# Kernel tuning notes

Measured on AMD Instinct MI355X. Metric: run time of the kernel, lower is better.

Reference implementation:

```python
import jax, jax.numpy as jnp
import numpy as np

E, T, D = 100000, 400000, 128
LN_EPS = 1e-5


def setup_inputs() -> dict:
    key = jax.random.key(0)
    k1, k2, k3 = jax.random.split(key, 3)
    f_edge = jax.random.normal(k1, (E, D), dtype=jnp.float32)
    W = jax.random.normal(k2, (3 * D, D), dtype=jnp.float32) / np.sqrt(3 * D)
    b = jnp.zeros((D,), dtype=jnp.float32)
    gamma = jnp.ones((D,), dtype=jnp.float32)
    beta = jnp.zeros((D,), dtype=jnp.float32)
    triangle = jax.random.randint(k3, (T, 3), 0, E, dtype=jnp.int64)
    return {"f_edge": f_edge, "W": W, "b": b, "gamma": gamma, "beta": beta,
            "triangle": triangle}


def reference(f_edge, W, b, gamma, beta, triangle):
    # f_edge [E, D], triangle [T, 3] -> gather to [T, 3, D], flatten to [T, 3D]
    t = triangle.shape[0]
    e, d = f_edge.shape
    f_tri = f_edge[triangle].reshape(t, 3 * d)
    # Linear(3D -> D) + exact GELU (torch nn.GELU default is erf-based)
    h = jax.nn.gelu(f_tri @ W + b, approximate=False)  # [T, D]
    # scatter_mean over destination edge index triangle[:, 2], dim_size=E
    dst = triangle[:, 2]
    seg_sum = jax.ops.segment_sum(h, dst, num_segments=e)            # [E, D]
    cnt = jax.ops.segment_sum(jnp.ones((t,), h.dtype), dst, num_segments=e)
    mean = seg_sum / jnp.maximum(cnt, 1.0)[:, None]
    # dropout is identity in eval mode; LayerNorm over last dim
    mu = jnp.mean(mean, axis=-1, keepdims=True)
    var = jnp.mean(jnp.square(mean - mu), axis=-1, keepdims=True)
    return (mean - mu) / jnp.sqrt(var + LN_EPS) * gamma + beta
```

## Files before the change

### kernel.cpp

```cpp
#include <hip/hip_runtime.h>
#include <hip/hip_bf16.h>

typedef __attribute__((ext_vector_type(8))) short short8;
typedef __attribute__((ext_vector_type(4))) float floatx4;
typedef __attribute__((ext_vector_type(4))) unsigned int uintx4;

__device__ __forceinline__ float gelu_fast(float x)
{
    float u = 0.7978845608f * x * (1.0f + 0.044715f * x * x);
    float e = __builtin_amdgcn_exp2f(2.885390082f * u);
    return x - x * __builtin_amdgcn_rcpf(e + 1.0f);
}

__global__ __launch_bounds__(256)
void prep(const float* __restrict__ Wg, uintx4* __restrict__ wq,
          const int* __restrict__ tri, int* __restrict__ cnt,
          int* __restrict__ slot, int T)
{
    int g = blockIdx.x * 256 + threadIdx.x;
    if (g < T) {
        int i2 = tri[g * 3 + 2];
        slot[g] = atomicAdd(&cnt[i2], 1);
    } else {
        int i = g - T;
        if (i < 6144) {
            int frag = i >> 6, lane = i & 63;
            int ko = frag >> 3, nt = frag & 7;
            int col = lane & 15, quad = lane >> 4;
            unsigned short tmp[8] __attribute__((aligned(16)));
#pragma unroll
            for (int j = 0; j < 8; ++j) {
                __hip_bfloat16 b =
                    __float2bfloat16(Wg[(ko * 32 + quad * 8 + j) * 128 + nt * 16 + col]);
                tmp[j] = *(unsigned short*)&b;
            }
            wq[i] = *(const uintx4*)tmp;
        }
    }
}

__device__ __forceinline__ int wave_incl_scan(int v, int lane)
{
#pragma unroll
    for (int o = 1; o < 64; o <<= 1) {
        int u = __shfl_up(v, o);
        if (lane >= o) v += u;
    }
    return v;
}

__global__ __launch_bounds__(1024)
void scan_blk(const int* __restrict__ in, int* __restrict__ outExcl,
              int* __restrict__ partial, int n,
              int* __restrict__ hist, int* __restrict__ histx)
{
    __shared__ int ws[16];
    __shared__ int lh[64];
    int t = threadIdx.x;
    int g = blockIdx.x * 1024 + t;
    int lane = t & 63, wv = t >> 6;
    int v = (g < n) ? in[g] : 0;
    int sc = wave_incl_scan(v, lane);
    if (lane == 63) ws[wv] = sc;
    if (hist && !histx && t < 64) lh[t] = 0;
    __syncthreads();
    if (wv == 0) {
        int b = (lane < 16) ? ws[lane] : 0;
        int bs = wave_incl_scan(b, lane);
        if (lane < 16) ws[lane] = bs;
    }
    if (hist && !histx && g < n) atomicAdd(&lh[v < 63 ? v : 63], 1);
    __syncthreads();
    int off = wv ? ws[wv - 1] : 0;
    if (g < n) outExcl[g] = off + sc - v;
    if (partial && t == 0) partial[blockIdx.x] = ws[15];
    if (hist && !histx && t < 64 && lh[t]) atomicAdd(&hist[t], lh[t]);
    if (histx && t < 64) {
        int hv = hist[t];
        int hs = wave_incl_scan(hv, lane);
        histx[t] = hs - hv;
    }
}

__global__ __launch_bounds__(256)
void scatter(const int* __restrict__ tri, const int* __restrict__ slot,
             const int* __restrict__ excl, const int* __restrict__ pscan,
             const int* __restrict__ cnt, int2* __restrict__ srec,
             const int* __restrict__ histx, int* __restrict__ histcur,
             int2* __restrict__ sinfo, int E, int T)
{
    __shared__ int lcnt[64];
    __shared__ int lbase[64];
    int t = threadIdx.x;
    int g = blockIdx.x * 256 + t;

    if (t < 64) lcnt[t] = 0;
    __syncthreads();

    int cc = 0, lofs = 0, c = 0, start = 0;
    if (g < E) {
        c = cnt[g];
        start = excl[g] + pscan[g >> 10];
        cc = c < 63 ? c : 63;
        lofs = atomicAdd(&lcnt[cc], 1);
    }
    __syncthreads();
    if (t < 64 && lcnt[t]) lbase[t] = atomicAdd(&histcur[t], lcnt[t]);
    __syncthreads();
    if (g < E) {
        int rank = histx[cc] + lbase[cc] + lofs;
        sinfo[rank] = make_int2((start << 8) | (c < 255 ? c : 255), g);
    }

    if (g < T) {
        int i0 = tri[g * 3 + 0];
        int i1 = tri[g * 3 + 1];
        int i2 = tri[g * 3 + 2];
        int pos = excl[i2] + pscan[i2 >> 10] + slot[g];
        srec[pos] = make_int2(i0 << 8, i1 << 8);
    }
    if (g < 8)
        srec[T + g] = make_int2(0, 0);
}

__global__ __launch_bounds__(1024, 1)
void edge_gemm(const float* __restrict__ fe_f, const uintx4* __restrict__ wq,
               unsigned short* __restrict__ G, int E)
{
    __shared__ uintx4 ldsW[6144];

    const int tid  = threadIdx.x;
    const int wv   = tid >> 6;
    const int lane = tid & 63;
    const int col  = lane & 15;
    const int quad = lane >> 4;
    const int ntiles = (E + 15) >> 4;

    for (int i = tid; i < 6144; i += 1024) ldsW[i] = wq[i];
    __syncthreads();

#pragma unroll 1
    for (int tile = blockIdx.x * 16 + wv; tile < ntiles; tile += gridDim.x * 16) {
        int row_a = tile * 16 + col;
        if (row_a >= E) row_a = E - 1;
        const float* arow = fe_f + (size_t)row_a * 128 + quad * 8;

        floatx4 f[8];
#pragma unroll
        for (int l = 0; l < 8; ++l)
            f[l] = *(const floatx4*)(arow + (l >> 1) * 32 + (l & 1) * 4);

        short8 a[4];
#pragma unroll
        for (int ko = 0; ko < 4; ++ko) {
            unsigned short tmp[8] __attribute__((aligned(16)));
#pragma unroll
            for (int j = 0; j < 8; ++j) {
                __hip_bfloat16 b = __float2bfloat16(f[ko * 2 + (j >> 2)][j & 3]);
                tmp[j] = *(unsigned short*)&b;
            }
            a[ko] = *(const short8*)tmp;
        }

#pragma unroll 1
        for (int r = 0; r < 3; ++r) {
            floatx4 acc[8];
#pragma unroll
            for (int nt = 0; nt < 8; ++nt) acc[nt] = (floatx4)0.0f;

#pragma unroll
            for (int ko = 0; ko < 4; ++ko) {
#pragma unroll
                for (int nt = 0; nt < 8; ++nt) {
                    short8 bf = *(const short8*)&ldsW[r * 2048 + (ko * 8 + nt) * 64 + lane];
                    acc[nt] = __builtin_amdgcn_mfma_f32_16x16x32_bf16(a[ko], bf, acc[nt], 0, 0, 0);
                }
            }

            unsigned short* Gr = G + (size_t)r * E * 128;
#pragma unroll
            for (int rr = 0; rr < 4; ++rr) {
                int row = tile * 16 + quad * 4 + rr;
                if (row < E) {
                    unsigned short pk[8] __attribute__((aligned(16)));
#pragma unroll
                    for (int nt = 0; nt < 8; ++nt) {
                        __hip_bfloat16 hb = __float2bfloat16(acc[nt][rr]);
                        pk[nt] = *(unsigned short*)&hb;
                    }
                    *(uintx4*)(Gr + (size_t)row * 128 + col * 8) = *(const uintx4*)pk;
                }
            }
        }
    }
}

__global__ __launch_bounds__(256)
void mean_ln(const unsigned short* __restrict__ G, const int2* __restrict__ sinfo,
             const int* __restrict__ cnt, const int2* __restrict__ srec,
             const float* __restrict__ bias, const float* __restrict__ gamma,
             const float* __restrict__ beta, float* __restrict__ out, int E)
{
    const int tid  = threadIdx.x;
    const int lane = tid & 63;
    const int wid  = tid >> 6;
    const int h    = lane >> 4;
    const int s    = lane & 15;

    const char* g0 = (const char*)G + s * 16;
    const char* g1 = g0 + (size_t)E * 256;
    const char* g2 = g1 + (size_t)E * 256;

    float bv[8], gm[8], bt[8];
#pragma unroll
    for (int k = 0; k < 8; ++k) {
        bv[k] = bias[k * 16 + s];
        gm[k] = gamma[k * 16 + s];
        bt[k] = beta[k * 16 + s];
    }

    const int ngroups = (E + 3) >> 2;
    const int nwaves  = gridDim.x * 4;

    for (int grp = blockIdx.x * 4 + wid; grp < ngroups; grp += nwaves) {
        int rank = grp * 4 + h;
        int rk   = rank < E ? rank : E - 1;

        int2 si  = sinfo[rk];
        int row  = si.y;
        int c    = si.x & 255;
        int start = (int)((unsigned)si.x >> 8);
        if (__builtin_expect(c == 255, 0)) c = cnt[row];

        int cmax = max(c, __shfl_xor(c, 16));
        cmax = max(cmax, __shfl_xor(cmax, 32));

        uintx4 w2 = *(const uintx4*)(g2 + (size_t)row * 256);
        float base[8];
#pragma unroll
        for (int k = 0; k < 8; ++k) {
            unsigned int wv = (k & 1) ? (w2[k >> 1] & 0xffff0000u)
                                      : (w2[k >> 1] << 16);
            base[k] = __uint_as_float(wv) + bv[k];
        }

        float x[8];
#pragma unroll
        for (int k = 0; k < 8; ++k) x[k] = 0.0f;

        int cl = c - 1; if (cl < 0) cl = 0;
        for (int t = 0; t < cmax; t += 4) {
            int ci = t + (s & 3);
            if (ci > cl) ci = cl;
            int2 rr = srec[start + ci];
#pragma unroll
            for (int k = 0; k < 4; ++k) {
                unsigned int o0 = (unsigned)__shfl(rr.x, (h << 4) + k);
                unsigned int o1 = (unsigned)__shfl(rr.y, (h << 4) + k);
                uintx4 a = *(const uintx4*)(g0 + (size_t)o0);
                uintx4 b = *(const uintx4*)(g1 + (size_t)o1);
                bool ok = (t + k) < c;
#pragma unroll
                for (int p = 0; p < 8; ++p) {
                    unsigned int wa = (p & 1) ? (a[p >> 1] & 0xffff0000u)
                                              : (a[p >> 1] << 16);
                    unsigned int wb = (p & 1) ? (b[p >> 1] & 0xffff0000u)
                                              : (b[p >> 1] << 16);
                    float sv = __uint_as_float(wa) + __uint_as_float(wb) + base[p];
                    x[p] += ok ? gelu_fast(sv) : 0.0f;
                }
            }
        }

        float inv = 1.0f / fmaxf((float)c, 1.0f);
        float sm = 0.0f;
#pragma unroll
        for (int k = 0; k < 8; ++k) { x[k] *= inv; sm += x[k]; }
#pragma unroll
        for (int o = 8; o > 0; o >>= 1) sm += __shfl_xor(sm, o);
        float mu = sm * (1.0f / 128.0f);
        float vv = 0.0f;
#pragma unroll
        for (int k = 0; k < 8; ++k) { x[k] -= mu; vv += x[k] * x[k]; }
#pragma unroll
        for (int o = 8; o > 0; o >>= 1) vv += __shfl_xor(vv, o);
        float rstd = rsqrtf(vv * (1.0f / 128.0f) + 1e-5f);

        if (rank < E) {
            float* orow = out + (size_t)row * 128 + s;
#pragma unroll
            for (int k = 0; k < 8; ++k)
                __builtin_nontemporal_store(x[k] * rstd * gm[k] + bt[k],
                                            &orow[k * 16]);
        }
    }
}

extern "C" void kernel_launch(void* const* d_in, const int* in_sizes, int n_in,
                              void* d_out, int out_size, void* d_ws, size_t ws_size,
                              hipStream_t stream)
{
    const float* fe_f  = (const float*)d_in[0];
    const float* Wg    = (const float*)d_in[1];
    const float* bias  = (const float*)d_in[2];
    const float* gamma = (const float*)d_in[3];
    const float* beta  = (const float*)d_in[4];
    const int*   tri   = (const int*)d_in[5];

    int E = in_sizes[0] / 128;
    int T = in_sizes[5] / 3;

    unsigned short* G = (unsigned short*)d_ws;
    int2* srec = (int2*)((char*)d_ws + (size_t)3 * E * 256);
    uintx4* wq = (uintx4*)(srec + T + 8);
    int* slot = (int*)(wq + 6144);
    int* cnt  = slot + T;
    int* hist = cnt + E;
    int* histcur = hist + 64;
    int* histx = histcur + 64;
    int* excl = histx + 64;
    int* partial = excl + E;
    int* pscan = partial + 1024;
    int2* sinfo = (int2*)(pscan + 1024);

    (void)hipMemsetAsync(cnt, 0, (size_t)E * sizeof(int) + 128 * sizeof(int),
                         stream);

    int total = T + 6144;
    prep<<<(total + 255) / 256, 256, 0, stream>>>(Wg, wq, tri, cnt, slot, T);

    int NB = (E + 1023) / 1024;
    scan_blk<<<NB, 1024, 0, stream>>>(cnt, excl, partial, E, hist, nullptr);
    scan_blk<<<1, 1024, 0, stream>>>(partial, pscan, nullptr, NB, hist, histx);

    scatter<<<(T + 255) / 256, 256, 0, stream>>>(tri, slot, excl, pscan, cnt,
                                                 srec, histx, histcur, sinfo,
                                                 E, T);

    edge_gemm<<<256, 1024, 0, stream>>>(fe_f, wq, G, E);

    mean_ln<<<2048, 256, 0, stream>>>(G, sinfo, cnt, srec, bias, gamma, beta,
                                      (float*)d_out, E);
}
```

Measured before the change: 209.5 us.

## Fuse scatter and second-level scan into GEMM launch as extra blocks

Drops the single-block partial-scan kernel and the separate scatter kernel. Their work now runs as extra blocks of the edge GEMM launch, and each of those blocks redoes the small partial and histogram scans locally. This removes two launches and lets the memory-bound scatter overlap with the MFMA-bound GEMM blocks. mean_ln also prefetches the next sinfo entry one iteration ahead and replaces the masked select with an FMA by a 0/1 mask. The cost is redundant small scans in every scatter block and a shared LDS footprint between the two roles.

```diff
diff --git a/kernel.cpp b/kernel.cpp
--- a/kernel.cpp
+++ b/kernel.cpp
@@ -4,6 +4,8 @@
 typedef __attribute__((ext_vector_type(8))) short short8;
 typedef __attribute__((ext_vector_type(4))) float floatx4;
 typedef __attribute__((ext_vector_type(4))) unsigned int uintx4;
+
+#define GEMM_BLOCKS 256
 
 __device__ __forceinline__ float gelu_fast(float x)
 {
@@ -51,8 +53,7 @@
 
 __global__ __launch_bounds__(1024)
 void scan_blk(const int* __restrict__ in, int* __restrict__ outExcl,
-              int* __restrict__ partial, int n,
-              int* __restrict__ hist, int* __restrict__ histx)
+              int* __restrict__ partial, int n, int* __restrict__ hist)
 {
     __shared__ int ws[16];
     __shared__ int lh[64];
@@ -62,136 +63,151 @@
     int v = (g < n) ? in[g] : 0;
     int sc = wave_incl_scan(v, lane);
     if (lane == 63) ws[wv] = sc;
-    if (hist && !histx && t < 64) lh[t] = 0;
+    if (t < 64) lh[t] = 0;
     __syncthreads();
     if (wv == 0) {
         int b = (lane < 16) ? ws[lane] : 0;
         int bs = wave_incl_scan(b, lane);
         if (lane < 16) ws[lane] = bs;
     }
-    if (hist && !histx && g < n) atomicAdd(&lh[v < 63 ? v : 63], 1);
+    if (g < n) atomicAdd(&lh[v < 63 ? v : 63], 1);
     __syncthreads();
     int off = wv ? ws[wv - 1] : 0;
     if (g < n) outExcl[g] = off + sc - v;
-    if (partial && t == 0) partial[blockIdx.x] = ws[15];
-    if (hist && !histx && t < 64 && lh[t]) atomicAdd(&hist[t], lh[t]);
-    if (histx && t < 64) {
-        int hv = hist[t];
-        int hs = wave_incl_scan(hv, lane);
-        histx[t] = hs - hv;
-    }
-}
-
-__global__ __launch_bounds__(256)
-void scatter(const int* __restrict__ tri, const int* __restrict__ slot,
-             const int* __restrict__ excl, const int* __restrict__ pscan,
-             const int* __restrict__ cnt, int2* __restrict__ srec,
-             const int* __restrict__ histx, int* __restrict__ histcur,
-             int2* __restrict__ sinfo, int E, int T)
-{
+    if (t == 0) partial[blockIdx.x] = ws[15];
+    if (t < 64 && lh[t]) atomicAdd(&hist[t], lh[t]);
+}
+
+__global__ __launch_bounds__(1024, 1)
+void gemm_scatter(const float* __restrict__ fe_f, const uintx4* __restrict__ wq,
+                  unsigned short* __restrict__ G, const int* __restrict__ tri,
+                  const int* __restrict__ slot, const int* __restrict__ excl,
+                  const int* __restrict__ partial, const int* __restrict__ hist,
+                  int* __restrict__ histcur, const int* __restrict__ cnt,
+                  int2* __restrict__ srec, int2* __restrict__ sinfo,
+                  int E, int T, int NB)
+{
+    __shared__ uintx4 ldsW[6144];
+    __shared__ int ps[128];
+    __shared__ int hx[64];
+    __shared__ int ws[16];
     __shared__ int lcnt[64];
     __shared__ int lbase[64];
-    int t = threadIdx.x;
-    int g = blockIdx.x * 256 + t;
-
-    if (t < 64) lcnt[t] = 0;
-    __syncthreads();
-
-    int cc = 0, lofs = 0, c = 0, start = 0;
-    if (g < E) {
-        c = cnt[g];
-        start = excl[g] + pscan[g >> 10];
-        cc = c < 63 ? c : 63;
-        lofs = atomicAdd(&lcnt[cc], 1);
-    }
-    __syncthreads();
-    if (t < 64 && lcnt[t]) lbase[t] = atomicAdd(&histcur[t], lcnt[t]);
-    __syncthreads();
-    if (g < E) {
-        int rank = histx[cc] + lbase[cc] + lofs;
-        sinfo[rank] = make_int2((start << 8) | (c < 255 ? c : 255), g);
-    }
-
-    if (g < T) {
-        int i0 = tri[g * 3 + 0];
-        int i1 = tri[g * 3 + 1];
-        int i2 = tri[g * 3 + 2];
-        int pos = excl[i2] + pscan[i2 >> 10] + slot[g];
-        srec[pos] = make_int2(i0 << 8, i1 << 8);
-    }
-    if (g < 8)
-        srec[T + g] = make_int2(0, 0);
-}
-
-__global__ __launch_bounds__(1024, 1)
-void edge_gemm(const float* __restrict__ fe_f, const uintx4* __restrict__ wq,
-               unsigned short* __restrict__ G, int E)
-{
-    __shared__ uintx4 ldsW[6144];
-
-    const int tid  = threadIdx.x;
-    const int wv   = tid >> 6;
-    const int lane = tid & 63;
-    const int col  = lane & 15;
-    const int quad = lane >> 4;
-    const int ntiles = (E + 15) >> 4;
-
-    for (int i = tid; i < 6144; i += 1024) ldsW[i] = wq[i];
-    __syncthreads();
+
+    const int tid = threadIdx.x;
+
+    if (blockIdx.x < GEMM_BLOCKS) {
+        const int wv   = tid >> 6;
+        const int lane = tid & 63;
+        const int col  = lane & 15;
+        const int quad = lane >> 4;
+        const int ntiles = (E + 15) >> 4;
+
+        for (int i = tid; i < 6144; i += 1024) ldsW[i] = wq[i];
+        __syncthreads();
 
 #pragma unroll 1
-    for (int tile = blockIdx.x * 16 + wv; tile < ntiles; tile += gridDim.x * 16) {
-        int row_a = tile * 16 + col;
-        if (row_a >= E) row_a = E - 1;
-        const float* arow = fe_f + (size_t)row_a * 128 + quad * 8;
-
-        floatx4 f[8];
-#pragma unroll
-        for (int l = 0; l < 8; ++l)
-            f[l] = *(const floatx4*)(arow + (l >> 1) * 32 + (l & 1) * 4);
-
-        short8 a[4];
-#pragma unroll
-        for (int ko = 0; ko < 4; ++ko) {
-            unsigned short tmp[8] __attribute__((aligned(16)));
-#pragma unroll
-            for (int j = 0; j < 8; ++j) {
-                __hip_bfloat16 b = __float2bfloat16(f[ko * 2 + (j >> 2)][j & 3]);
-                tmp[j] = *(unsigned short*)&b;
+        for (int tile = blockIdx.x * 16 + wv; tile < ntiles;
+             tile += GEMM_BLOCKS * 16) {
+            int row_a = tile * 16 + col;
+            if (row_a >= E) row_a = E - 1;
+            const float* arow = fe_f + (size_t)row_a * 128 + quad * 8;
+
+            floatx4 f[8];
+#pragma unroll
+            for (int l = 0; l < 8; ++l)
+                f[l] = *(const floatx4*)(arow + (l >> 1) * 32 + (l & 1) * 4);
+
+            short8 a[4];
+#pragma unroll
+            for (int ko = 0; ko < 4; ++ko) {
+                unsigned short tmp[8] __attribute__((aligned(16)));
+#pragma unroll
+                for (int j = 0; j < 8; ++j) {
+                    __hip_bfloat16 b = __float2bfloat16(f[ko * 2 + (j >> 2)][j & 3]);
+                    tmp[j] = *(unsigned short*)&b;
+                }
+                a[ko] = *(const short8*)tmp;
             }
-            a[ko] = *(const short8*)tmp;
-        }
 
 #pragma unroll 1
-        for (int r = 0; r < 3; ++r) {
-            floatx4 acc[8];
-#pragma unroll
-            for (int nt = 0; nt < 8; ++nt) acc[nt] = (floatx4)0.0f;
-
-#pragma unroll
-            for (int ko = 0; ko < 4; ++ko) {
-#pragma unroll
-                for (int nt = 0; nt < 8; ++nt) {
-                    short8 bf = *(const short8*)&ldsW[r * 2048 + (ko * 8 + nt) * 64 + lane];
-                    acc[nt] = __builtin_amdgcn_mfma_f32_16x16x32_bf16(a[ko], bf, acc[nt], 0, 0, 0);
+            for (int r = 0; r < 3; ++r) {
+                floatx4 acc[8];
+#pragma unroll
+                for (int nt = 0; nt < 8; ++nt) acc[nt] = (floatx4)0.0f;
+
+#pragma unroll
+                for (int ko = 0; ko < 4; ++ko) {
+#pragma unroll
+                    for (int nt = 0; nt < 8; ++nt) {
+                        short8 bf = *(const short8*)&ldsW[r * 2048 + (ko * 8 + nt) * 64 + lane];
+                        acc[nt] = __builtin_amdgcn_mfma_f32_16x16x32_bf16(a[ko], bf, acc[nt], 0, 0, 0);
+                    }
+                }
+
+                unsigned short* Gr = G + (size_t)r * E * 128;
+#pragma unroll
+                for (int rr = 0; rr < 4; ++rr) {
+                    int row = tile * 16 + quad * 4 + rr;
+                    if (row < E) {
+                        unsigned short pk[8] __attribute__((aligned(16)));
+#pragma unroll
+                        for (int nt = 0; nt < 8; ++nt) {
+                            __hip_bfloat16 hb = __float2bfloat16(acc[nt][rr]);
+                            pk[nt] = *(unsigned short*)&hb;
+                        }
+                        *(uintx4*)(Gr + (size_t)row * 128 + col * 8) = *(const uintx4*)pk;
+                    }
                 }
             }
-
-            unsigned short* Gr = G + (size_t)r * E * 128;
-#pragma unroll
-            for (int rr = 0; rr < 4; ++rr) {
-                int row = tile * 16 + quad * 4 + rr;
-                if (row < E) {
-                    unsigned short pk[8] __attribute__((aligned(16)));
-#pragma unroll
-                    for (int nt = 0; nt < 8; ++nt) {
-                        __hip_bfloat16 hb = __float2bfloat16(acc[nt][rr]);
-                        pk[nt] = *(unsigned short*)&hb;
-                    }
-                    *(uintx4*)(Gr + (size_t)row * 128 + col * 8) = *(const uintx4*)pk;
-                }
-            }
-        }
+        }
+    } else {
+        const int lane = tid & 63, w = tid >> 6;
+
+        int v = (tid < NB) ? partial[tid] : 0;
+        int sc = wave_incl_scan(v, lane);
+        if (lane == 63) ws[w] = sc;
+        if (tid < 64) lcnt[tid] = 0;
+        __syncthreads();
+        if (w == 0) {
+            int b = (lane < 16) ? ws[lane] : 0;
+            int bs = wave_incl_scan(b, lane);
+            if (lane < 16) ws[lane] = bs;
+            int hv = hist[lane];
+            int hs = wave_incl_scan(hv, lane);
+            hx[lane] = hs - hv;
+        }
+        __syncthreads();
+        int off = w ? ws[w - 1] : 0;
+        if (tid < NB && tid < 128) ps[tid] = off + sc - v;
+        __syncthreads();
+
+        int g = (blockIdx.x - GEMM_BLOCKS) * 1024 + tid;
+
+        int cc = 0, lofs = 0, c = 0, start = 0;
+        if (g < E) {
+            c = cnt[g];
+            start = excl[g] + ps[g >> 10];
+            cc = c < 63 ? c : 63;
+            lofs = atomicAdd(&lcnt[cc], 1);
+        }
+        __syncthreads();
+        if (tid < 64 && lcnt[tid]) lbase[tid] = atomicAdd(&histcur[tid], lcnt[tid]);
+        __syncthreads();
+        if (g < E) {
+            int rank = hx[cc] + lbase[cc] + lofs;
+            sinfo[rank] = make_int2((start << 8) | (c < 255 ? c : 255), g);
+        }
+
+        if (g < T) {
+            int i0 = tri[g * 3 + 0];
+            int i1 = tri[g * 3 + 1];
+            int i2 = tri[g * 3 + 2];
+            int pos = excl[i2] + ps[i2 >> 10] + slot[g];
+            srec[pos] = make_int2(i0 << 8, i1 << 8);
+        }
+        if (g < 8)
+            srec[T + g] = make_int2(0, 0);
     }
 }
 
@@ -222,11 +238,19 @@
     const int ngroups = (E + 3) >> 2;
     const int nwaves  = gridDim.x * 4;
 
-    for (int grp = blockIdx.x * 4 + wid; grp < ngroups; grp += nwaves) {
+    int grp = blockIdx.x * 4 + wid;
+    if (grp >= ngroups) return;
+    int rk0 = grp * 4 + h;
+    if (rk0 >= E) rk0 = E - 1;
+    int2 si = sinfo[rk0];
+
+    for (; grp < ngroups; grp += nwaves) {
+        int gn = grp + nwaves;
+        int rkn = gn * 4 + h;
+        if (rkn >= E) rkn = E - 1;
+        int2 si_nx = (gn < ngroups) ? sinfo[rkn] : si;
+
         int rank = grp * 4 + h;
-        int rk   = rank < E ? rank : E - 1;
-
-        int2 si  = sinfo[rk];
         int row  = si.y;
         int c    = si.x & 255;
         int start = (int)((unsigned)si.x >> 8);
@@ -259,7 +283,7 @@
                 unsigned int o1 = (unsigned)__shfl(rr.y, (h << 4) + k);
                 uintx4 a = *(const uintx4*)(g0 + (size_t)o0);
                 uintx4 b = *(const uintx4*)(g1 + (size_t)o1);
-                bool ok = (t + k) < c;
+                float mk = (t + k) < c ? 1.0f : 0.0f;
 #pragma unroll
                 for (int p = 0; p < 8; ++p) {
                     unsigned int wa = (p & 1) ? (a[p >> 1] & 0xffff0000u)
@@ -267,7 +291,7 @@
                     unsigned int wb = (p & 1) ? (b[p >> 1] & 0xffff0000u)
                                               : (b[p >> 1] << 16);
                     float sv = __uint_as_float(wa) + __uint_as_float(wb) + base[p];
-                    x[p] += ok ? gelu_fast(sv) : 0.0f;
+                    x[p] = __builtin_fmaf(mk, gelu_fast(sv), x[p]);
                 }
             }
         }
@@ -293,6 +317,7 @@
                 __builtin_nontemporal_store(x[k] * rstd * gm[k] + bt[k],
                                             &orow[k * 16]);
         }
+        si = si_nx;
     }
 }
 
@@ -317,11 +342,9 @@
     int* cnt  = slot + T;
     int* hist = cnt + E;
     int* histcur = hist + 64;
-    int* histx = histcur + 64;
-    int* excl = histx + 64;
+    int* excl = histcur + 128;
     int* partial = excl + E;
-    int* pscan = partial + 1024;
-    int2* sinfo = (int2*)(pscan + 1024);
+    int2* sinfo = (int2*)(partial + 1024);
 
     (void)hipMemsetAsync(cnt, 0, (size_t)E * sizeof(int) + 128 * sizeof(int),
                          stream);
@@ -330,14 +353,12 @@
     prep<<<(total + 255) / 256, 256, 0, stream>>>(Wg, wq, tri, cnt, slot, T);
 
     int NB = (E + 1023) / 1024;
-    scan_blk<<<NB, 1024, 0, stream>>>(cnt, excl, partial, E, hist, nullptr);
-    scan_blk<<<1, 1024, 0, stream>>>(partial, pscan, nullptr, NB, hist, histx);
-
-    scatter<<<(T + 255) / 256, 256, 0, stream>>>(tri, slot, excl, pscan, cnt,
-                                                 srec, histx, histcur, sinfo,
-                                                 E, T);
-
-    edge_gemm<<<256, 1024, 0, stream>>>(fe_f, wq, G, E);
+    scan_blk<<<NB, 1024, 0, stream>>>(cnt, excl, partial, E, hist);
+
+    int SB = (T + 1023) / 1024;
+    gemm_scatter<<<GEMM_BLOCKS + SB, 1024, 0, stream>>>(
+        fe_f, wq, G, tri, slot, excl, partial, hist, histcur, cnt,
+        srec, sinfo, E, T, NB);
 
     mean_ln<<<2048, 256, 0, stream>>>(G, sinfo, cnt, srec, bias, gamma, beta,
                                       (float*)d_out, E);
```

Measured after the change: 200.7 us. -4.2%, faster.
